# Kernel tuning notes

Measured on AMD Instinct MI355X. Metric: run time of the kernel, lower is better.

The kernel has to match this reference:

```python
import jax, jax.numpy as jnp
import numpy as np

SIG = 10
C = 0.0
STD = 1.0
N_ATOMS = 21
N_TRAIN = 8192
DESC = N_ATOMS * (N_ATOMS - 1) // 2  # 210
M = 64


def setup_inputs() -> dict:
    key = jax.random.key(0)
    k1, k2, k3 = jax.random.split(key, 3)
    Rs = jax.random.normal(k1, (M, N_ATOMS, 3), dtype=jnp.float32)
    xs_train = jax.random.uniform(k2, (N_TRAIN, DESC), dtype=jnp.float32)
    Jx_alphas = jax.random.normal(k3, (N_TRAIN, DESC), dtype=jnp.float32)
    return {"Rs": Rs, "xs_train": xs_train, "Jx_alphas": Jx_alphas}


def reference(Rs, xs_train, Jx_alphas):
    sig = SIG
    q = np.sqrt(5.0) / sig
    n = N_ATOMS
    # pairwise atom displacements / distances: [M, n, n, 3], [M, n, n]
    diffs = Rs[:, :, None, :] - Rs[:, None, :, :]
    dists = jnp.linalg.norm(diffs, axis=-1)
    eye = jnp.eye(n, dtype=bool)
    dists = jnp.where(eye, jnp.inf, dists)  # kill diagonal
    i, j = np.tril_indices(n, k=-1)
    xs = 1.0 / dists[:, i, j]                       # [M, D] inverse-distance descriptor
    x_diffs = q * xs[:, None, :] - q * xs_train     # [M, T, D]
    x_dists = jnp.linalg.norm(x_diffs, axis=-1)     # [M, T]
    exp_xs = (5.0 / (3.0 * sig ** 2)) * jnp.exp(-x_dists)
    dot = jnp.einsum('mtd,td->mt', x_diffs, Jx_alphas)
    exp_xs_1 = exp_xs * (1.0 + x_dists)
    F1s_x = jnp.einsum('mt,mtd->md', exp_xs * dot, x_diffs)  # [M, D]
    F2s_x = exp_xs_1 @ Jx_alphas                              # [M, D]
    Fs_x = (F1s_x - F2s_x) * STD
    # expand_tril: scatter D lower-tri values to symmetric [M, n, n], zero diag
    full = jnp.zeros((Fs_x.shape[0], n, n), dtype=Fs_x.dtype)
    full = full.at[:, i, j].set(Fs_x).at[:, j, i].set(Fs_x)
    Fs = jnp.einsum('mab,mabc->mac', full / dists ** 3, diffs)  # diag: 0/inf -> 0
    Es = jnp.sum(exp_xs_1 * dot, axis=-1) / q
    Es = C + Es * STD
    return Es, Fs
```

## Files before the change

### kernel.cpp

```cpp
#include <hip/hip_runtime.h>
#include <math.h>

#define NA   21
#define NM   64
#define ND   210
#define DP   224
#define NT   8192
#define NCH  28
#define KS2  32

#define QC 0.22360679774997896f
#define KE 0.016666666666666666f

typedef short bf8 __attribute__((ext_vector_type(8)));
typedef float f4  __attribute__((ext_vector_type(4)));

#define O_XF   0u
#define O_JF   917504u
#define O_XFT  1835008u
#define O_JFT  2752512u
#define O_W1   3670016u
#define O_E1   3932160u
#define O_AF   4194304u
#define O_QG   4201472u
#define O_NTT  4215808u
#define O_CJ   4224000u
#define O_NX   4232192u
#define O_AB   4232384u
#define O_PB   4261056u
#define O_ESP  5178560u
#define O_WAP  5211328u

__device__ __forceinline__ unsigned short f2bf(float f) {
    unsigned u = __float_as_uint(f);
    u += 0x7fffu + ((u >> 16) & 1u);
    return (unsigned short)(u >> 16);
}
__device__ __forceinline__ float bf2f(unsigned short h) {
    return __uint_as_float((unsigned)h << 16);
}

__device__ __forceinline__ void d_to_ij(int d, int& i, int& j) {
    int ii = (int)((1.0f + sqrtf(1.0f + 8.0f * (float)d)) * 0.5f);
    while (ii * (ii - 1) / 2 > d) --ii;
    while ((ii + 1) * ii / 2 <= d) ++ii;
    i = ii;
    j = d - ii * (ii - 1) / 2;
}

__global__ __launch_bounds__(256) void k_prep(
    const float* __restrict__ Rs, const float* __restrict__ xs,
    const float* __restrict__ Jx,
    unsigned short* __restrict__ Xf, unsigned short* __restrict__ Jf,
    unsigned short* __restrict__ XfT, unsigned short* __restrict__ JfT,
    unsigned short* __restrict__ Af, float* __restrict__ qxsG,
    float* __restrict__ nx, float* __restrict__ nt, float* __restrict__ cJ) {
    const int b = blockIdx.x, tid = threadIdx.x;
    __shared__ float lds[64 * 210];

    if (b < 512) {
        const int t0 = b * 16;
        const float4* sx = (const float4*)(xs + (size_t)t0 * ND);
        const float4* sj = (const float4*)(Jx + (size_t)t0 * ND);
#pragma unroll
        for (int k = 0; k < 4; ++k) {
            const int i = k * 256 + tid;
            if (i < 840) {
                ((float4*)lds)[i] = sx[i];
                ((float4*)(lds + 3360))[i] = sj[i];
            }
        }
        __syncthreads();
#pragma unroll
        for (int k = 0; k < 4; ++k) {
            const int idx = k * 256 + tid;
            if (idx < 896) {
                const int arr = idx / 448;
                const int rem = idx - arr * 448;
                const int kq = rem >> 4, colt = rem & 15;
                const float* src = lds + arr * 3360 + colt * 210;
                const float sc = arr ? 1.0f : QC;
                union { unsigned short us[8]; uint4 v; } u;
#pragma unroll
                for (int i = 0; i < 8; ++i) {
                    const int d = kq * 8 + i;
                    u.us[i] = (d < ND) ? f2bf(sc * src[d]) : (unsigned short)0;
                }
                *(uint4*)((arr ? Jf : Xf) + ((size_t)(b * NCH + kq) * 16 + colt) * 8) = u.v;
            }
        }
        const int tt = tid >> 4, l = tid & 15;
        const float* xr = lds + tt * 210;
        const float* jr = lds + 3360 + tt * 210;
        float sn = 0.0f, sc2 = 0.0f;
        for (int c = l; c < ND; c += 16) {
            float x = bf2f(f2bf(QC * xr[c]));
            float j = bf2f(f2bf(jr[c]));
            sn = fmaf(x, x, sn);
            sc2 = fmaf(x, j, sc2);
        }
#pragma unroll
        for (int off = 1; off < 16; off <<= 1) {
            sn += __shfl_xor(sn, off);
            sc2 += __shfl_xor(sc2, off);
        }
        if (l == 0) {
            nt[t0 + tt] = sn;
            cJ[t0 + tt] = sc2;
        }
    } else if (b < 768) {
        const int bb = b - 512;
        const int arr = bb >> 7;
        const int tpos = bb & 127;
        const int t0 = tpos * 64;
        const float4* s = (const float4*)((arr ? Jx : xs) + (size_t)t0 * ND);
#pragma unroll
        for (int k = 0; k < 14; ++k) {
            const int i = k * 256 + tid;
            if (i < 3360) ((float4*)lds)[i] = s[i];
        }
        __syncthreads();
        unsigned short* dst = arr ? JfT : XfT;
        const float sc = arr ? 1.0f : QC;
#pragma unroll
        for (int k = 0; k < 7; ++k) {
            const int idx = k * 256 + tid;
            const int dtile = idx >> 7;
            const int rem = idx & 127;
            const int tql = rem >> 4, col = rem & 15;
            const int d = dtile * 16 + col;
            union { unsigned short us[8]; uint4 v; } u;
#pragma unroll
            for (int i = 0; i < 8; ++i)
                u.us[i] = (d < ND) ? f2bf(sc * lds[(tql * 8 + i) * 210 + d])
                                   : (unsigned short)0;
            *(uint4*)(dst + ((size_t)(dtile * 1024 + tpos * 8 + tql) * 16 + col) * 8) = u.v;
        }
    } else {
        const int m = b - 768;
        float* R = lds;
        float* red = lds + 64;
        if (tid < NA * 3) R[tid] = Rs[m * NA * 3 + tid];
        __syncthreads();
        float local = 0.0f;
        if (tid < DP) {
            float vr = 0.0f;
            unsigned short hv = 0;
            if (tid < ND) {
                int i, j; d_to_ij(tid, i, j);
                float dx = R[i * 3] - R[j * 3];
                float dy = R[i * 3 + 1] - R[j * 3 + 1];
                float dz = R[i * 3 + 2] - R[j * 3 + 2];
                float v = QC / sqrtf(dx * dx + dy * dy + dz * dz);
                hv = f2bf(v);
                vr = bf2f(hv);
            }
            Af[(((m >> 4) * NCH + (tid >> 3)) * 16 + (m & 15)) * 8 + (tid & 7)] = hv;
            qxsG[(tid >> 2) * 256 + m * 4 + (tid & 3)] = vr;
            local = vr * vr;
        }
        red[tid] = local;
        __syncthreads();
        for (int s = 128; s > 0; s >>= 1) {
            if (tid < s) red[tid] += red[tid + s];
            __syncthreads();
        }
        if (tid == 0) nx[m] = red[0];
    }
}

__global__ __launch_bounds__(256) void k_stage1(
    const unsigned short* __restrict__ Af, const unsigned short* __restrict__ Xf,
    const unsigned short* __restrict__ Jf, const float* __restrict__ nt,
    const float* __restrict__ cJ, const float* __restrict__ nx,
    unsigned short* __restrict__ w1f, unsigned short* __restrict__ e1f,
    float* __restrict__ EsPart, float* __restrict__ WaPart) {
    const int tid = threadIdx.x;
    const int lane = tid & 63;
    const int w = tid >> 6;
    const int col = lane & 15, quad = lane >> 4;
    const int ttile = blockIdx.x;
    __shared__ float Dw[64][17];
    __shared__ float De[64][17];

    const unsigned short* ap = Af + ((size_t)(w * NCH + quad) * 16 + col) * 8;
    const unsigned short* xp = Xf + ((size_t)(ttile * NCH + quad) * 16 + col) * 8;
    const unsigned short* jp = Jf + ((size_t)(ttile * NCH + quad) * 16 + col) * 8;

    bf8 af[7];
#pragma unroll
    for (int kc = 0; kc < 7; ++kc) af[kc] = *(const bf8*)(ap + kc * 512);

    bf8 bx[2], bj[2];
    bx[0] = *(const bf8*)xp;
    bj[0] = *(const bf8*)jp;
    bx[1] = *(const bf8*)(xp + 512);
    bj[1] = *(const bf8*)(jp + 512);

    f4 c1 = {0.f, 0.f, 0.f, 0.f};
    f4 c2 = {0.f, 0.f, 0.f, 0.f};
#pragma unroll
    for (int kc = 0; kc < 7; ++kc) {
        const int s = kc & 1;
        c1 = __builtin_amdgcn_mfma_f32_16x16x32_bf16(af[kc], bx[s], c1, 0, 0, 0);
        c2 = __builtin_amdgcn_mfma_f32_16x16x32_bf16(af[kc], bj[s], c2, 0, 0, 0);
        if (kc < 5) {
            bx[s] = *(const bf8*)(xp + (kc + 2) * 512);
            bj[s] = *(const bf8*)(jp + (kc + 2) * 512);
        }
    }

    const int t = ttile * 16 + col;
    const float ntv = nt[t], cjv = cJ[t];
    float esA[4], wlA[4];
#pragma unroll
    for (int r = 0; r < 4; ++r) {
        const int m = w * 16 + quad * 4 + r;
        float sq = fmaxf(nx[m] - 2.0f * c1[r] + ntv, 0.0f);
        float xd = sqrtf(sq);
        float e = KE * expf(-xd);
        float dotv = c2[r] - cjv;
        float wv = e * dotv;
        float ev = e * (1.0f + xd);
        Dw[m][col] = wv;
        De[m][col] = ev;
        esA[r] = ev * dotv;
        wlA[r] = wv;
    }
    __syncthreads();
    {
        const int aidx = tid >> 7;
        const int c = tid & 127;
        const int mtile = c >> 5, tql = (c >> 4) & 1, colm = c & 15;
        const float* srcD = aidx ? &De[0][0] : &Dw[0][0];
        unsigned short* dst = aidx ? e1f : w1f;
        const int m = mtile * 16 + colm;
        union { unsigned short us[8]; uint4 v; } u;
#pragma unroll
        for (int i = 0; i < 8; ++i) u.us[i] = f2bf(srcD[m * 17 + tql * 8 + i]);
        const size_t off = ((size_t)(mtile * 1024 + ttile * 2 + tql) * 16 + colm) * 8;
        *(uint4*)(dst + off) = u.v;
    }
#pragma unroll
    for (int r = 0; r < 4; ++r) {
        float e = esA[r], wl = wlA[r];
#pragma unroll
        for (int off = 1; off < 16; off <<= 1) {
            e += __shfl_xor(e, off);
            wl += __shfl_xor(wl, off);
        }
        if (col == 0) {
            const int m = w * 16 + quad * 4 + r;
            EsPart[(size_t)m * 512 + ttile] = e;
            WaPart[(size_t)m * 512 + ttile] = wl;
        }
    }
}

__global__ __launch_bounds__(256) void k_stage2(
    const unsigned short* __restrict__ w1f, const unsigned short* __restrict__ e1f,
    const unsigned short* __restrict__ XfT, const unsigned short* __restrict__ JfT,
    float* __restrict__ Pbuf) {
    const int tid = threadIdx.x;
    const int lane = tid & 63;
    const int w = tid >> 6;
    const int col = lane & 15, quad = lane >> 4;
    const int dt = blockIdx.x;
    const int by = blockIdx.y;

    const unsigned short* awp = w1f + ((size_t)(w * 1024 + by * 32 + quad) * 16 + col) * 8;
    const unsigned short* aep = e1f + ((size_t)(w * 1024 + by * 32 + quad) * 16 + col) * 8;
    const unsigned short* bxp = XfT + ((size_t)(dt * 1024 + by * 32 + quad) * 16 + col) * 8;
    const unsigned short* bjp = JfT + ((size_t)(dt * 1024 + by * 32 + quad) * 16 + col) * 8;

    bf8 aw[2], ae[2], bx[2], bj[2];
    aw[0] = *(const bf8*)awp;         ae[0] = *(const bf8*)aep;
    bx[0] = *(const bf8*)bxp;         bj[0] = *(const bf8*)bjp;
    aw[1] = *(const bf8*)(awp + 512); ae[1] = *(const bf8*)(aep + 512);
    bx[1] = *(const bf8*)(bxp + 512); bj[1] = *(const bf8*)(bjp + 512);

    f4 dA = {0.f, 0.f, 0.f, 0.f};
    f4 dB = {0.f, 0.f, 0.f, 0.f};
#pragma unroll
    for (int kk = 0; kk < 8; ++kk) {
        const int s = kk & 1;
        dA = __builtin_amdgcn_mfma_f32_16x16x32_bf16(aw[s], bx[s], dA, 0, 0, 0);
        dB = __builtin_amdgcn_mfma_f32_16x16x32_bf16(ae[s], bj[s], dB, 0, 0, 0);
        if (kk < 6) {
            aw[s] = *(const bf8*)(awp + (kk + 2) * 512);
            ae[s] = *(const bf8*)(aep + (kk + 2) * 512);
            bx[s] = *(const bf8*)(bxp + (kk + 2) * 512);
            bj[s] = *(const bf8*)(bjp + (kk + 2) * 512);
        }
    }
    float* p = Pbuf + (size_t)by * 28672 + dt * 16 + col;
#pragma unroll
    for (int r = 0; r < 4; ++r) {
        const int m = w * 16 + quad * 4 + r;
        p[m * DP] = dA[r];
        p[14336 + m * DP] = dB[r];
    }
}

__global__ void k_reduce(const float* __restrict__ P, float* __restrict__ AB) {
    const int o = blockIdx.x * 256 + threadIdx.x;
    float s = 0.0f;
#pragma unroll 8
    for (int ks = 0; ks < KS2; ++ks) s += P[(size_t)ks * 28672 + o];
    AB[o] = s;
}

__global__ void k_final(const float* __restrict__ Rs, const float* __restrict__ qxsG,
                        const float* __restrict__ AB, const float* __restrict__ EsPart,
                        const float* __restrict__ WaPart, float* __restrict__ out) {
    int m = blockIdx.x, tid = threadIdx.x;
    __shared__ float R[NA * 3];
    __shared__ float Ff[NA][NA];
    __shared__ float redE[256];
    __shared__ float redW[256];
    if (tid < NA * 3) R[tid] = Rs[m * NA * 3 + tid];
    if (tid < NA) Ff[tid][tid] = 0.0f;
    {
        const float2 ep = ((const float2*)(EsPart + (size_t)m * 512))[tid];
        const float2 wp = ((const float2*)(WaPart + (size_t)m * 512))[tid];
        redE[tid] = ep.x + ep.y;
        redW[tid] = wp.x + wp.y;
    }
    __syncthreads();
    for (int s = 128; s > 0; s >>= 1) {
        if (tid < s) {
            redE[tid] += redE[tid + s];
            redW[tid] += redW[tid + s];
        }
        __syncthreads();
    }
    const float Wa = redW[0];
    if (tid < ND) {
        int i, j; d_to_ij(tid, i, j);
        float dx = R[i * 3] - R[j * 3];
        float dy = R[i * 3 + 1] - R[j * 3 + 1];
        float dz = R[i * 3 + 2] - R[j * 3 + 2];
        float dist2 = dx * dx + dy * dy + dz * dz;
        float fsx = qxsG[(tid >> 2) * 256 + m * 4 + (tid & 3)] * Wa
                  - AB[(size_t)m * DP + tid]
                  - AB[14336 + (size_t)m * DP + tid];
        float f = fsx / (dist2 * sqrtf(dist2));
        Ff[i][j] = f;
        Ff[j][i] = f;
    }
    __syncthreads();
    if (tid < NA * 3) {
        int a = tid / 3, c = tid % 3;
        float s = 0.0f;
        for (int b = 0; b < NA; ++b) {
            if (b == a) continue;
            s += Ff[a][b] * (R[a * 3 + c] - R[b * 3 + c]);
        }
        out[NM + m * NA * 3 + tid] = s;
    }
    if (tid == 0) out[m] = redE[0] / QC;
}

extern "C" void kernel_launch(void* const* d_in, const int* in_sizes, int n_in,
                              void* d_out, int out_size, void* d_ws, size_t ws_size,
                              hipStream_t stream) {
    const float* Rs = (const float*)d_in[0];
    const float* xs_train = (const float*)d_in[1];
    const float* Jx_alphas = (const float*)d_in[2];
    float* out = (float*)d_out;
    float* ws = (float*)d_ws;

    unsigned short* Xf  = (unsigned short*)(ws + O_XF);
    unsigned short* Jf  = (unsigned short*)(ws + O_JF);
    unsigned short* XfT = (unsigned short*)(ws + O_XFT);
    unsigned short* JfT = (unsigned short*)(ws + O_JFT);
    unsigned short* w1f = (unsigned short*)(ws + O_W1);
    unsigned short* e1f = (unsigned short*)(ws + O_E1);
    unsigned short* Af  = (unsigned short*)(ws + O_AF);
    float* qxsG   = ws + O_QG;
    float* nt     = ws + O_NTT;
    float* cJ     = ws + O_CJ;
    float* nx     = ws + O_NX;
    float* ABf    = ws + O_AB;
    float* Pbuf   = ws + O_PB;
    float* EsPart = ws + O_ESP;
    float* WaPart = ws + O_WAP;

    k_prep<<<832, 256, 0, stream>>>(Rs, xs_train, Jx_alphas, Xf, Jf, XfT, JfT,
                                    Af, qxsG, nx, nt, cJ);
    k_stage1<<<512, 256, 0, stream>>>(Af, Xf, Jf, nt, cJ, nx, w1f, e1f, EsPart, WaPart);
    k_stage2<<<dim3(14, KS2), 256, 0, stream>>>(w1f, e1f, XfT, JfT, Pbuf);
    k_reduce<<<112, 256, 0, stream>>>(Pbuf, ABf);
    k_final<<<NM, 256, 0, stream>>>(Rs, qxsG, ABf, EsPart, WaPart, out);
}
```

Before: 92.20 us.

## Fuse transposed-layout prep into tile blocks and fold split-K reduce into final

The transposed bf16 copies (XfT/JfT) are now written by the same prep blocks that already load each 16-row tile into LDS. This drops the separate 256 blocks that re-read xs_train and Jx_alphas from global memory. The k_reduce launch is removed, and k_final sums the 32 split-K partials for both products directly into shared memory. This saves one kernel launch and an AB round-trip. In exchange, k_final does 64 strided global loads per thread across only 64 blocks, and the prep blocks do more work each.

```diff
diff --git a/kernel.cpp b/kernel.cpp
--- a/kernel.cpp
+++ b/kernel.cpp
@@ -26,7 +26,6 @@
 #define O_NTT  4215808u
 #define O_CJ   4224000u
 #define O_NX   4232192u
-#define O_AB   4232384u
 #define O_PB   4261056u
 #define O_ESP  5178560u
 #define O_WAP  5211328u
@@ -56,7 +55,7 @@
     unsigned short* __restrict__ Af, float* __restrict__ qxsG,
     float* __restrict__ nx, float* __restrict__ nt, float* __restrict__ cJ) {
     const int b = blockIdx.x, tid = threadIdx.x;
-    __shared__ float lds[64 * 210];
+    __shared__ float lds[2 * 16 * 210];
 
     if (b < 512) {
         const int t0 = b * 16;
@@ -72,7 +71,7 @@
         }
         __syncthreads();
 #pragma unroll
-        for (int k = 0; k < 4; ++k) {
+        for (int k = 0; k < 7; ++k) {
             const int idx = k * 256 + tid;
             if (idx < 896) {
                 const int arr = idx / 448;
@@ -87,6 +86,23 @@
                     u.us[i] = (d < ND) ? f2bf(sc * src[d]) : (unsigned short)0;
                 }
                 *(uint4*)((arr ? Jf : Xf) + ((size_t)(b * NCH + kq) * 16 + colt) * 8) = u.v;
+            } else {
+                const int idx2 = idx - 896;
+                const int arr = idx2 / 448;
+                const int rem = idx2 - arr * 448;
+                const int dtile = rem >> 5;
+                const int rem2 = rem & 31;
+                const int tql = rem2 >> 4, col = rem2 & 15;
+                const int d = dtile * 16 + col;
+                const float* src = lds + arr * 3360 + tql * 8 * 210;
+                const float sc = arr ? 1.0f : QC;
+                union { unsigned short us[8]; uint4 v; } u;
+#pragma unroll
+                for (int i = 0; i < 8; ++i)
+                    u.us[i] = (d < ND) ? f2bf(sc * src[i * 210 + d])
+                                       : (unsigned short)0;
+                const size_t off = ((size_t)(dtile * 1024 + b * 2 + tql) * 16 + col) * 8;
+                *(uint4*)((arr ? JfT : XfT) + off) = u.v;
             }
         }
         const int tt = tid >> 4, l = tid & 15;
@@ -108,36 +124,8 @@
             nt[t0 + tt] = sn;
             cJ[t0 + tt] = sc2;
         }
-    } else if (b < 768) {
-        const int bb = b - 512;
-        const int arr = bb >> 7;
-        const int tpos = bb & 127;
-        const int t0 = tpos * 64;
-        const float4* s = (const float4*)((arr ? Jx : xs) + (size_t)t0 * ND);
-#pragma unroll
-        for (int k = 0; k < 14; ++k) {
-            const int i = k * 256 + tid;
-            if (i < 3360) ((float4*)lds)[i] = s[i];
-        }
-        __syncthreads();
-        unsigned short* dst = arr ? JfT : XfT;
-        const float sc = arr ? 1.0f : QC;
-#pragma unroll
-        for (int k = 0; k < 7; ++k) {
-            const int idx = k * 256 + tid;
-            const int dtile = idx >> 7;
-            const int rem = idx & 127;
-            const int tql = rem >> 4, col = rem & 15;
-            const int d = dtile * 16 + col;
-            union { unsigned short us[8]; uint4 v; } u;
-#pragma unroll
-            for (int i = 0; i < 8; ++i)
-                u.us[i] = (d < ND) ? f2bf(sc * lds[(tql * 8 + i) * 210 + d])
-                                   : (unsigned short)0;
-            *(uint4*)(dst + ((size_t)(dtile * 1024 + tpos * 8 + tql) * 16 + col) * 8) = u.v;
-        }
     } else {
-        const int m = b - 768;
+        const int m = b - 512;
         float* R = lds;
         float* red = lds + 64;
         if (tid < NA * 3) R[tid] = Rs[m * NA * 3 + tid];
@@ -302,24 +290,27 @@
     }
 }
 
-__global__ void k_reduce(const float* __restrict__ P, float* __restrict__ AB) {
-    const int o = blockIdx.x * 256 + threadIdx.x;
-    float s = 0.0f;
-#pragma unroll 8
-    for (int ks = 0; ks < KS2; ++ks) s += P[(size_t)ks * 28672 + o];
-    AB[o] = s;
-}
-
 __global__ void k_final(const float* __restrict__ Rs, const float* __restrict__ qxsG,
-                        const float* __restrict__ AB, const float* __restrict__ EsPart,
+                        const float* __restrict__ Pbuf, const float* __restrict__ EsPart,
                         const float* __restrict__ WaPart, float* __restrict__ out) {
     int m = blockIdx.x, tid = threadIdx.x;
     __shared__ float R[NA * 3];
     __shared__ float Ff[NA][NA];
     __shared__ float redE[256];
     __shared__ float redW[256];
+    __shared__ float ABs[DP];
     if (tid < NA * 3) R[tid] = Rs[m * NA * 3 + tid];
     if (tid < NA) Ff[tid][tid] = 0.0f;
+    if (tid < DP) {
+        const float* p0 = Pbuf + (size_t)m * DP + tid;
+        float s1 = 0.0f, s2 = 0.0f;
+#pragma unroll
+        for (int ks = 0; ks < KS2; ++ks) {
+            s1 += p0[(size_t)ks * 28672];
+            s2 += p0[(size_t)ks * 28672 + 14336];
+        }
+        ABs[tid] = s1 + s2;
+    }
     {
         const float2 ep = ((const float2*)(EsPart + (size_t)m * 512))[tid];
         const float2 wp = ((const float2*)(WaPart + (size_t)m * 512))[tid];
@@ -341,9 +332,7 @@
         float dy = R[i * 3 + 1] - R[j * 3 + 1];
         float dz = R[i * 3 + 2] - R[j * 3 + 2];
         float dist2 = dx * dx + dy * dy + dz * dz;
-        float fsx = qxsG[(tid >> 2) * 256 + m * 4 + (tid & 3)] * Wa
-                  - AB[(size_t)m * DP + tid]
-                  - AB[14336 + (size_t)m * DP + tid];
+        float fsx = qxsG[(tid >> 2) * 256 + m * 4 + (tid & 3)] * Wa - ABs[tid];
         float f = fsx / (dist2 * sqrtf(dist2));
         Ff[i][j] = f;
         Ff[j][i] = f;
@@ -381,15 +370,13 @@
     float* nt     = ws + O_NTT;
     float* cJ     = ws + O_CJ;
     float* nx     = ws + O_NX;
-    float* ABf    = ws + O_AB;
     float* Pbuf   = ws + O_PB;
     float* EsPart = ws + O_ESP;
     float* WaPart = ws + O_WAP;
 
-    k_prep<<<832, 256, 0, stream>>>(Rs, xs_train, Jx_alphas, Xf, Jf, XfT, JfT,
+    k_prep<<<576, 256, 0, stream>>>(Rs, xs_train, Jx_alphas, Xf, Jf, XfT, JfT,
                                     Af, qxsG, nx, nt, cJ);
     k_stage1<<<512, 256, 0, stream>>>(Af, Xf, Jf, nt, cJ, nx, w1f, e1f, EsPart, WaPart);
     k_stage2<<<dim3(14, KS2), 256, 0, stream>>>(w1f, e1f, XfT, JfT, Pbuf);
-    k_reduce<<<112, 256, 0, stream>>>(Pbuf, ABf);
-    k_final<<<NM, 256, 0, stream>>>(Rs, qxsG, ABf, EsPart, WaPart, out);
-}
+    k_final<<<NM, 256, 0, stream>>>(Rs, qxsG, Pbuf, EsPart, WaPart, out);
+}
```

Result: no change. 92.13 us, median of 2 (-0.1%).
